# Performance work log

Hardware: AMD Instinct MI355X
Metric: run time of the kernel (lower is better)

## Reference

```python
import jax, jax.numpy as jnp
import numpy as np

TEMPERATURE = 0.07


def setup_inputs() -> dict:
    key = jax.random.key(0)
    k1, k2 = jax.random.split(key)
    B, D = 8192, 256
    embeddings = jax.random.normal(k1, (B, D), dtype=jnp.float32)
    ids = jax.random.randint(k2, (B,), 0, 1024, dtype=jnp.int64 if jax.config.jax_enable_x64 else jnp.int32)
    return {"embeddings": embeddings, "ids": ids}


def reference(embeddings, ids):
    B = embeddings.shape[0]
    # L2-normalize rows (F.normalize with p=2, dim=1)
    emb = embeddings / jnp.maximum(jnp.linalg.norm(embeddings, axis=1, keepdims=True), 1e-12)
    sim = (emb @ emb.T) / TEMPERATURE                      # [B, B]
    eye = jnp.eye(B, dtype=bool)
    sim = jnp.where(eye, -jnp.inf, sim)
    exp_sim = jnp.exp(sim)                                  # diag -> 0
    pos_mask = (ids[:, None] == ids[None, :]) & ~eye        # [B, B]
    pos_sum = jnp.sum(jnp.where(pos_mask, exp_sim, 0.0), axis=1)  # [B]
    all_sum = jnp.sum(exp_sim, axis=1)                      # [B]
    valid = pos_mask.any(axis=1)
    per_row = -jnp.log(pos_sum / all_sum)
    loss = jnp.sum(jnp.where(valid, per_row, 0.0))
    n_valid = jnp.sum(valid.astype(jnp.float32))
    return loss / jnp.maximum(n_valid, 1.0)
```

## Files before the change

### kernel.cpp

```cpp
#include <hip/hip_runtime.h>
#include <hip/hip_bf16.h>

#define B_SZ 8192
#define D_SZ 256
#define NTILES 2080
#define GRID_SIM 512
#define PRESCALE 4.539816004686735f

typedef __attribute__((ext_vector_type(4))) float f32x4;
typedef __attribute__((ext_vector_type(8))) short s16x8;

__global__ __launch_bounds__(256) void norm_kernel(const float* __restrict__ emb,
                                                   ushort* __restrict__ nbf,
                                                   float* __restrict__ sums) {
    sums[blockIdx.x * 64 + (threadIdx.x >> 2)] = 0.0f;

    const int wave = threadIdx.x >> 6, lane = threadIdx.x & 63;
    for (int g = blockIdx.x; g < B_SZ / 4; g += 256) {
        const int row = g * 4 + wave;
        const float4 v = ((const float4*)(emb + (size_t)row * D_SZ))[lane];
        float ss = v.x * v.x + v.y * v.y + v.z * v.z + v.w * v.w;
        #pragma unroll
        for (int m = 1; m < 64; m <<= 1) ss += __shfl_xor(ss, m, 64);
        float s = PRESCALE / fmaxf(sqrtf(ss), 1e-12f);
        __hip_bfloat16 b0 = __float2bfloat16(v.x * s);
        __hip_bfloat16 b1 = __float2bfloat16(v.y * s);
        __hip_bfloat16 b2 = __float2bfloat16(v.z * s);
        __hip_bfloat16 b3 = __float2bfloat16(v.w * s);
        ushort4 o;
        o.x = *(ushort*)&b0; o.y = *(ushort*)&b1; o.z = *(ushort*)&b2; o.w = *(ushort*)&b3;
        ((ushort4*)(nbf + (size_t)row * D_SZ))[lane] = o;
    }
}

__device__ __forceinline__ void decode_tile(int tb, int& i0, int& j0, bool& diag) {
    int bj = (int)((sqrtf(8.0f * tb + 1.0f) - 1.0f) * 0.5f);
    while ((bj + 1) * (bj + 2) / 2 <= tb) ++bj;
    while (bj * (bj + 1) / 2 > tb) --bj;
    const int bi = tb - bj * (bj + 1) / 2;
    i0 = bi * 128; j0 = bj * 128; diag = (bi == bj);
}

__device__ __forceinline__ void load_regs(s16x8 ra[4], s16x8 rb[4],
                                          const ushort* __restrict__ N,
                                          int i0, int j0, int k0,
                                          int wave, int r, int c8s) {
    const ushort* gA = N + (size_t)(i0 + wave * 32) * D_SZ + k0;
    const ushort* gB = N + (size_t)(j0 + wave * 32) * D_SZ + k0;
    #pragma unroll
    for (int q = 0; q < 4; ++q) {
        ra[q] = *(const s16x8*)(gA + (size_t)(q * 8 + r) * D_SZ + c8s);
        rb[q] = *(const s16x8*)(gB + (size_t)(q * 8 + r) * D_SZ + c8s);
    }
}

__device__ __forceinline__ void store_stage(const s16x8 ra[4], const s16x8 rb[4],
                                            ushort* bA, ushort* bB,
                                            int wave, int lane) {
    #pragma unroll
    for (int q = 0; q < 4; ++q) {
        *(s16x8*)&bA[(wave * 32 + q * 8) * 64 + lane * 8] = ra[q];
        *(s16x8*)&bB[(wave * 32 + q * 8) * 64 + lane * 8] = rb[q];
    }
}

__global__ __launch_bounds__(256) void sim_kernel(const ushort* __restrict__ N,
                                                  const int* __restrict__ ids,
                                                  float* __restrict__ all_sum,
                                                  float* __restrict__ pos_sum) {
    __shared__ ushort smem[4 * 128 * 64];

    const int t    = threadIdx.x;
    const int wave = t >> 6, lane = t & 63;
    const int wy   = wave >> 1, wx = wave & 1;
    const int r    = lane >> 3;
    const int c8s  = ((lane & 7) ^ r) * 8;
    const int myc  = lane & 15;

    int tb = blockIdx.x;
    int i0, j0; bool diag;
    decode_tile(tb, i0, j0, diag);

    s16x8 ra[4], rb[4];
    load_regs(ra, rb, N, i0, j0, 0, wave, r, c8s);

    while (true) {
        const int ntb = tb + GRID_SIM;
        const bool have_next = (ntb < NTILES);
        int ni0 = i0, nj0 = j0; bool ndiag = diag;
        if (have_next) decode_tile(ntb, ni0, nj0, ndiag);

        f32x4 acc[4][4];
        #pragma unroll
        for (int mi = 0; mi < 4; ++mi)
            #pragma unroll
            for (int ni = 0; ni < 4; ++ni)
                acc[mi][ni] = (f32x4){0.f, 0.f, 0.f, 0.f};

        #pragma unroll
        for (int kk = 0; kk < 4; ++kk) {
            ushort* bA = smem + (kk & 1) * 16384;
            ushort* bB = bA + 8192;
            store_stage(ra, rb, bA, bB, wave, lane);
            if (kk < 3)           load_regs(ra, rb, N, i0, j0, (kk + 1) * 64, wave, r, c8s);
            else if (have_next)   load_regs(ra, rb, N, ni0, nj0, 0, wave, r, c8s);
            __syncthreads();

            #pragma unroll
            for (int ks = 0; ks < 2; ++ks) {
                const int C = ks * 4 + (lane >> 4);
                const int slot = (C ^ (lane & 7)) * 8;
                s16x8 af[4], bf[4];
                #pragma unroll
                for (int mi = 0; mi < 4; ++mi)
                    af[mi] = *(const s16x8*)&bA[(wy * 64 + mi * 16 + (lane & 15)) * 64 + slot];
                #pragma unroll
                for (int ni = 0; ni < 4; ++ni)
                    bf[ni] = *(const s16x8*)&bB[(wx * 64 + ni * 16 + (lane & 15)) * 64 + slot];
                #pragma unroll
                for (int mi = 0; mi < 4; ++mi)
                    #pragma unroll
                    for (int ni = 0; ni < 4; ++ni)
                        acc[mi][ni] = __builtin_amdgcn_mfma_f32_16x16x32_bf16(
                            af[mi], bf[ni], acc[mi][ni], 0, 0, 0);
            }
        }

        float* rowAllPart = (float*)smem;
        float* rowPosPart = (float*)&smem[8192];

        int idc[4];
        #pragma unroll
        for (int ni = 0; ni < 4; ++ni)
            idc[ni] = ids[j0 + wx * 64 + ni * 16 + myc];

        float cAll[4] = {0.f, 0.f, 0.f, 0.f};
        float cPos[4] = {0.f, 0.f, 0.f, 0.f};

        #pragma unroll
        for (int mi = 0; mi < 4; ++mi) {
            float rAll[4] = {0.f, 0.f, 0.f, 0.f};
            float rPos[4] = {0.f, 0.f, 0.f, 0.f};
            const int rbase = wy * 64 + mi * 16 + (lane >> 4) * 4;
            const int4 idr  = *(const int4*)&ids[i0 + rbase];
            #pragma unroll
            for (int ni = 0; ni < 4; ++ni) {
                const int cloc = wx * 64 + ni * 16 + myc;
                #pragma unroll
                for (int rg = 0; rg < 4; ++rg) {
                    const int lr = rbase + rg;
                    float e = __builtin_amdgcn_exp2f(acc[mi][ni][rg]);
                    if (diag && lr == cloc) e = 0.0f;
                    rAll[rg] += e; cAll[ni] += e;
                    const int idrv = (rg == 0) ? idr.x : (rg == 1) ? idr.y
                                   : (rg == 2) ? idr.z : idr.w;
                    if (idrv == idc[ni]) { rPos[rg] += e; cPos[ni] += e; }
                }
            }
            #pragma unroll
            for (int rg = 0; rg < 4; ++rg) {
                rowAllPart[(rbase + rg) * 32 + wx * 16 + myc] = rAll[rg];
                rowPosPart[(rbase + rg) * 32 + wx * 16 + myc] = rPos[rg];
            }
        }

        if (!diag) {
            #pragma unroll
            for (int ni = 0; ni < 4; ++ni) {
                cAll[ni] += __shfl_xor(cAll[ni], 16, 64);
                cAll[ni] += __shfl_xor(cAll[ni], 32, 64);
                cPos[ni] += __shfl_xor(cPos[ni], 16, 64);
                cPos[ni] += __shfl_xor(cPos[ni], 32, 64);
            }
            if (lane < 16) {
                #pragma unroll
                for (int ni = 0; ni < 4; ++ni) {
                    const int gc = j0 + wx * 64 + ni * 16 + lane;
                    atomicAdd(&all_sum[gc], cAll[ni]);
                    if (cPos[ni] != 0.0f) atomicAdd(&pos_sum[gc], cPos[ni]);
                }
            }
        }

        __syncthreads();
        {
            const int row = t & 127;
            const float* src = (t >= 128) ? rowPosPart : rowAllPart;
            float s = 0.0f;
            #pragma unroll
            for (int k8 = 0; k8 < 8; ++k8) {
                const int chunk = (k8 + (row & 7)) & 7;
                const float4 v = *(const float4*)&src[row * 32 + chunk * 4];
                s += v.x + v.y + v.z + v.w;
            }
            float* dst = (t >= 128) ? pos_sum : all_sum;
            atomicAdd(&dst[i0 + row], s);
        }
        __syncthreads();

        if (!have_next) break;
        tb = ntb; i0 = ni0; j0 = nj0; diag = ndiag;
    }
}

__global__ __launch_bounds__(256) void loss_kernel(const float* __restrict__ all_sum,
                                                   const float* __restrict__ pos_sum,
                                                   float* __restrict__ out) {
    float loss = 0.0f, cnt = 0.0f;
    for (int i = threadIdx.x; i < B_SZ; i += 256) {
        float p = pos_sum[i], a = all_sum[i];
        if (p > 0.0f) { loss += logf(a) - logf(p); cnt += 1.0f; }
    }
    #pragma unroll
    for (int m = 1; m < 64; m <<= 1) {
        loss += __shfl_xor(loss, m, 64);
        cnt  += __shfl_xor(cnt, m, 64);
    }
    __shared__ float sl[4], sc[4];
    int wave = threadIdx.x >> 6, lane = threadIdx.x & 63;
    if (lane == 0) { sl[wave] = loss; sc[wave] = cnt; }
    __syncthreads();
    if (threadIdx.x == 0) {
        float L = sl[0] + sl[1] + sl[2] + sl[3];
        float C = sc[0] + sc[1] + sc[2] + sc[3];
        out[0] = L / fmaxf(C, 1.0f);
    }
}

extern "C" void kernel_launch(void* const* d_in, const int* in_sizes, int n_in,
                              void* d_out, int out_size, void* d_ws, size_t ws_size,
                              hipStream_t stream) {
    const float* emb = (const float*)d_in[0];
    const int*   ids = (const int*)d_in[1];
    float*       out = (float*)d_out;

    float*  all_sum = (float*)d_ws;
    float*  pos_sum = all_sum + B_SZ;
    ushort* nbf     = (ushort*)((char*)d_ws + 65536);

    norm_kernel<<<256, 256, 0, stream>>>(emb, nbf, all_sum);
    sim_kernel<<<GRID_SIM, 256, 0, stream>>>(nbf, ids, all_sum, pos_sum);
    loss_kernel<<<1, 256, 0, stream>>>(all_sum, pos_sum, out);
}
```

Before: 117.4 us.

## Shrink LDS stages to 32-wide K, deepen prefetch, and reduce rows via shuffles

The K loop now runs as eight 32-wide stages over a smaller double-buffered LDS region with a two-deep register prefetch, using a new XOR swizzle. The row-sum epilogue drops the LDS staging and its two block barriers; rows are instead reduced with wave shuffles and atomics from each half-wave. The grid doubles to 1024 blocks so more tiles run concurrently now that LDS use is lower. The cost is twice as many barriers per tile and more global atomics on the row sums.

Measured after the change: 182.4 us. 55.3% more time.

```diff
diff --git a/kernel.cpp b/kernel.cpp
--- a/kernel.cpp
+++ b/kernel.cpp
@@ -4,7 +4,7 @@
 #define B_SZ 8192
 #define D_SZ 256
 #define NTILES 2080
-#define GRID_SIM 512
+#define GRID_SIM 1024
 #define PRESCALE 4.539816004686735f
 
 typedef __attribute__((ext_vector_type(4))) float f32x4;
@@ -41,48 +41,74 @@
     i0 = bi * 128; j0 = bj * 128; diag = (bi == bj);
 }
 
-__device__ __forceinline__ void load_regs(s16x8 ra[4], s16x8 rb[4],
-                                          const ushort* __restrict__ N,
-                                          int i0, int j0, int k0,
-                                          int wave, int r, int c8s) {
-    const ushort* gA = N + (size_t)(i0 + wave * 32) * D_SZ + k0;
-    const ushort* gB = N + (size_t)(j0 + wave * 32) * D_SZ + k0;
-    #pragma unroll
-    for (int q = 0; q < 4; ++q) {
-        ra[q] = *(const s16x8*)(gA + (size_t)(q * 8 + r) * D_SZ + c8s);
-        rb[q] = *(const s16x8*)(gB + (size_t)(q * 8 + r) * D_SZ + c8s);
-    }
-}
-
-__device__ __forceinline__ void store_stage(const s16x8 ra[4], const s16x8 rb[4],
-                                            ushort* bA, ushort* bB,
-                                            int wave, int lane) {
-    #pragma unroll
-    for (int q = 0; q < 4; ++q) {
-        *(s16x8*)&bA[(wave * 32 + q * 8) * 64 + lane * 8] = ra[q];
-        *(s16x8*)&bB[(wave * 32 + q * 8) * 64 + lane * 8] = rb[q];
-    }
+__device__ __forceinline__ void load32(int4 ra[2], int4 rb[2],
+                                       const ushort* __restrict__ N,
+                                       int i0, int j0, int ke,
+                                       int wave, int lane) {
+    const int rbase = wave * 16 + (lane >> 2);
+    const int g     = lane & 3;
+    #pragma unroll
+    for (int h = 0; h < 2; ++h) {
+        const int row = rbase + h * 64;
+        ra[h] = *(const int4*)(N + (size_t)(i0 + row) * D_SZ + ke + g * 8);
+        rb[h] = *(const int4*)(N + (size_t)(j0 + row) * D_SZ + ke + g * 8);
+    }
+}
+
+__device__ __forceinline__ void store32(const int4 ra[2], const int4 rb[2],
+                                        ushort* bufA, ushort* bufB,
+                                        int wave, int lane) {
+    const int rbase = wave * 16 + (lane >> 2);
+    const int g     = lane & 3;
+    #pragma unroll
+    for (int h = 0; h < 2; ++h) {
+        const int row = rbase + h * 64;
+        const int s   = g ^ ((row >> 1) & 3);
+        *(int4*)&bufA[row * 32 + s * 8] = ra[h];
+        *(int4*)&bufB[row * 32 + s * 8] = rb[h];
+    }
+}
+
+__device__ __forceinline__ void compute32(const ushort* bufA, const ushort* bufB,
+                                          f32x4 acc[4][4], int wy, int wx, int lane) {
+    const int c16 = lane >> 4;
+    s16x8 af[4], bf[4];
+    #pragma unroll
+    for (int mi = 0; mi < 4; ++mi) {
+        const int rr = wy * 64 + mi * 16 + (lane & 15);
+        af[mi] = *(const s16x8*)&bufA[rr * 32 + (c16 ^ ((rr >> 1) & 3)) * 8];
+    }
+    #pragma unroll
+    for (int ni = 0; ni < 4; ++ni) {
+        const int rr = wx * 64 + ni * 16 + (lane & 15);
+        bf[ni] = *(const s16x8*)&bufB[rr * 32 + (c16 ^ ((rr >> 1) & 3)) * 8];
+    }
+    #pragma unroll
+    for (int mi = 0; mi < 4; ++mi)
+        #pragma unroll
+        for (int ni = 0; ni < 4; ++ni)
+            acc[mi][ni] = __builtin_amdgcn_mfma_f32_16x16x32_bf16(
+                af[mi], bf[ni], acc[mi][ni], 0, 0, 0);
 }
 
 __global__ __launch_bounds__(256) void sim_kernel(const ushort* __restrict__ N,
                                                   const int* __restrict__ ids,
                                                   float* __restrict__ all_sum,
                                                   float* __restrict__ pos_sum) {
-    __shared__ ushort smem[4 * 128 * 64];
+    __shared__ ushort smem[2 * 2 * 128 * 32];
 
     const int t    = threadIdx.x;
     const int wave = t >> 6, lane = t & 63;
     const int wy   = wave >> 1, wx = wave & 1;
-    const int r    = lane >> 3;
-    const int c8s  = ((lane & 7) ^ r) * 8;
     const int myc  = lane & 15;
 
     int tb = blockIdx.x;
     int i0, j0; bool diag;
     decode_tile(tb, i0, j0, diag);
 
-    s16x8 ra[4], rb[4];
-    load_regs(ra, rb, N, i0, j0, 0, wave, r, c8s);
+    int4 ra[2][2], rb[2][2];
+    load32(ra[0], rb[0], N, i0, j0, 0,  wave, lane);
+    load32(ra[1], rb[1], N, i0, j0, 32, wave, lane);
 
     while (true) {
         const int ntb = tb + GRID_SIM;
@@ -98,36 +124,18 @@
                 acc[mi][ni] = (f32x4){0.f, 0.f, 0.f, 0.f};
 
         #pragma unroll
-        for (int kk = 0; kk < 4; ++kk) {
-            ushort* bA = smem + (kk & 1) * 16384;
-            ushort* bB = bA + 8192;
-            store_stage(ra, rb, bA, bB, wave, lane);
-            if (kk < 3)           load_regs(ra, rb, N, i0, j0, (kk + 1) * 64, wave, r, c8s);
-            else if (have_next)   load_regs(ra, rb, N, ni0, nj0, 0, wave, r, c8s);
+        for (int kk = 0; kk < 8; ++kk) {
+            ushort* bufA = smem + (kk & 1) * 8192;
+            ushort* bufB = bufA + 4096;
+            const int s = kk & 1;
+            store32(ra[s], rb[s], bufA, bufB, wave, lane);
+            if (kk + 2 < 8)
+                load32(ra[s], rb[s], N, i0, j0, (kk + 2) * 32, wave, lane);
+            else if (have_next)
+                load32(ra[s], rb[s], N, ni0, nj0, (kk + 2 - 8) * 32, wave, lane);
             __syncthreads();
-
-            #pragma unroll
-            for (int ks = 0; ks < 2; ++ks) {
-                const int C = ks * 4 + (lane >> 4);
-                const int slot = (C ^ (lane & 7)) * 8;
-                s16x8 af[4], bf[4];
-                #pragma unroll
-                for (int mi = 0; mi < 4; ++mi)
-                    af[mi] = *(const s16x8*)&bA[(wy * 64 + mi * 16 + (lane & 15)) * 64 + slot];
-                #pragma unroll
-                for (int ni = 0; ni < 4; ++ni)
-                    bf[ni] = *(const s16x8*)&bB[(wx * 64 + ni * 16 + (lane & 15)) * 64 + slot];
-                #pragma unroll
-                for (int mi = 0; mi < 4; ++mi)
-                    #pragma unroll
-                    for (int ni = 0; ni < 4; ++ni)
-                        acc[mi][ni] = __builtin_amdgcn_mfma_f32_16x16x32_bf16(
-                            af[mi], bf[ni], acc[mi][ni], 0, 0, 0);
-            }
+            compute32(bufA, bufB, acc, wy, wx, lane);
         }
-
-        float* rowAllPart = (float*)smem;
-        float* rowPosPart = (float*)&smem[8192];
 
         int idc[4];
         #pragma unroll
@@ -148,9 +156,8 @@
                 const int cloc = wx * 64 + ni * 16 + myc;
                 #pragma unroll
                 for (int rg = 0; rg < 4; ++rg) {
-                    const int lr = rbase + rg;
                     float e = __builtin_amdgcn_exp2f(acc[mi][ni][rg]);
-                    if (diag && lr == cloc) e = 0.0f;
+                    if (diag && (rbase + rg) == cloc) e = 0.0f;
                     rAll[rg] += e; cAll[ni] += e;
                     const int idrv = (rg == 0) ? idr.x : (rg == 1) ? idr.y
                                    : (rg == 2) ? idr.z : idr.w;
@@ -159,8 +166,18 @@
             }
             #pragma unroll
             for (int rg = 0; rg < 4; ++rg) {
-                rowAllPart[(rbase + rg) * 32 + wx * 16 + myc] = rAll[rg];
-                rowPosPart[(rbase + rg) * 32 + wx * 16 + myc] = rPos[rg];
+                #pragma unroll
+                for (int mm = 1; mm < 16; mm <<= 1) {
+                    rAll[rg] += __shfl_xor(rAll[rg], mm, 64);
+                    rPos[rg] += __shfl_xor(rPos[rg], mm, 64);
+                }
+            }
+            if (myc == 0) {
+                #pragma unroll
+                for (int rg = 0; rg < 4; ++rg) {
+                    atomicAdd(&all_sum[i0 + rbase + rg], rAll[rg]);
+                    if (rPos[rg] != 0.0f) atomicAdd(&pos_sum[i0 + rbase + rg], rPos[rg]);
+                }
             }
         }
 
@@ -181,22 +198,6 @@
                 }
             }
         }
-
-        __syncthreads();
-        {
-            const int row = t & 127;
-            const float* src = (t >= 128) ? rowPosPart : rowAllPart;
-            float s = 0.0f;
-            #pragma unroll
-            for (int k8 = 0; k8 < 8; ++k8) {
-                const int chunk = (k8 + (row & 7)) & 7;
-                const float4 v = *(const float4*)&src[row * 32 + chunk * 4];
-                s += v.x + v.y + v.z + v.w;
-            }
-            float* dst = (t >= 128) ? pos_sum : all_sum;
-            atomicAdd(&dst[i0 + row], s);
-        }
-        __syncthreads();
 
         if (!have_next) break;
         tb = ntb; i0 = ni0; j0 = nj0; diag = ndiag;
```

## Single-buffer LDS, reduce row sums with shuffles, and double the grid

Applied to the files above, without the earlier changes.

Replaces the double-buffered shared memory with single A/B buffers plus an extra barrier per k-step, halving LDS use so more blocks can be resident. Row partial sums are now reduced with intra-wave shuffles and atomically added directly, instead of going through a shared-memory transpose and a second reduction pass with two barriers. The grid size doubles to 1024 to take advantage of the higher occupancy. The cost is an added sync per k-step and twice as many global atomics on row sums (one per wave-column half).

Result: slower. 130.5 us (+11.1%).

```diff
diff --git a/kernel.cpp b/kernel.cpp
--- a/kernel.cpp
+++ b/kernel.cpp
@@ -4,7 +4,7 @@
 #define B_SZ 8192
 #define D_SZ 256
 #define NTILES 2080
-#define GRID_SIM 512
+#define GRID_SIM 1024
 #define PRESCALE 4.539816004686735f
 
 typedef __attribute__((ext_vector_type(4))) float f32x4;
@@ -68,7 +68,8 @@
                                                   const int* __restrict__ ids,
                                                   float* __restrict__ all_sum,
                                                   float* __restrict__ pos_sum) {
-    __shared__ ushort smem[4 * 128 * 64];
+    __shared__ ushort sA[128 * 64];
+    __shared__ ushort sB[128 * 64];
 
     const int t    = threadIdx.x;
     const int wave = t >> 6, lane = t & 63;
@@ -99,9 +100,8 @@
 
         #pragma unroll
         for (int kk = 0; kk < 4; ++kk) {
-            ushort* bA = smem + (kk & 1) * 16384;
-            ushort* bB = bA + 8192;
-            store_stage(ra, rb, bA, bB, wave, lane);
+            __syncthreads();
+            store_stage(ra, rb, sA, sB, wave, lane);
             if (kk < 3)           load_regs(ra, rb, N, i0, j0, (kk + 1) * 64, wave, r, c8s);
             else if (have_next)   load_regs(ra, rb, N, ni0, nj0, 0, wave, r, c8s);
             __syncthreads();
@@ -113,10 +113,10 @@
                 s16x8 af[4], bf[4];
                 #pragma unroll
                 for (int mi = 0; mi < 4; ++mi)
-                    af[mi] = *(const s16x8*)&bA[(wy * 64 + mi * 16 + (lane & 15)) * 64 + slot];
+                    af[mi] = *(const s16x8*)&sA[(wy * 64 + mi * 16 + (lane & 15)) * 64 + slot];
                 #pragma unroll
                 for (int ni = 0; ni < 4; ++ni)
-                    bf[ni] = *(const s16x8*)&bB[(wx * 64 + ni * 16 + (lane & 15)) * 64 + slot];
+                    bf[ni] = *(const s16x8*)&sB[(wx * 64 + ni * 16 + (lane & 15)) * 64 + slot];
                 #pragma unroll
                 for (int mi = 0; mi < 4; ++mi)
                     #pragma unroll
@@ -126,9 +126,6 @@
             }
         }
 
-        float* rowAllPart = (float*)smem;
-        float* rowPosPart = (float*)&smem[8192];
-
         int idc[4];
         #pragma unroll
         for (int ni = 0; ni < 4; ++ni)
@@ -148,9 +145,8 @@
                 const int cloc = wx * 64 + ni * 16 + myc;
                 #pragma unroll
                 for (int rg = 0; rg < 4; ++rg) {
-                    const int lr = rbase + rg;
                     float e = __builtin_amdgcn_exp2f(acc[mi][ni][rg]);
-                    if (diag && lr == cloc) e = 0.0f;
+                    if (diag && (rbase + rg) == cloc) e = 0.0f;
                     rAll[rg] += e; cAll[ni] += e;
                     const int idrv = (rg == 0) ? idr.x : (rg == 1) ? idr.y
                                    : (rg == 2) ? idr.z : idr.w;
@@ -159,8 +155,18 @@
             }
             #pragma unroll
             for (int rg = 0; rg < 4; ++rg) {
-                rowAllPart[(rbase + rg) * 32 + wx * 16 + myc] = rAll[rg];
-                rowPosPart[(rbase + rg) * 32 + wx * 16 + myc] = rPos[rg];
+                #pragma unroll
+                for (int mm = 1; mm < 16; mm <<= 1) {
+                    rAll[rg] += __shfl_xor(rAll[rg], mm, 64);
+                    rPos[rg] += __shfl_xor(rPos[rg], mm, 64);
+                }
+            }
+            if (myc == 0) {
+                #pragma unroll
+                for (int rg = 0; rg < 4; ++rg) {
+                    atomicAdd(&all_sum[i0 + rbase + rg], rAll[rg]);
+                    if (rPos[rg] != 0.0f) atomicAdd(&pos_sum[i0 + rbase + rg], rPos[rg]);
+                }
             }
         }
 
@@ -181,22 +187,6 @@
                 }
             }
         }
-
-        __syncthreads();
-        {
-            const int row = t & 127;
-            const float* src = (t >= 128) ? rowPosPart : rowAllPart;
-            float s = 0.0f;
-            #pragma unroll
-            for (int k8 = 0; k8 < 8; ++k8) {
-                const int chunk = (k8 + (row & 7)) & 7;
-                const float4 v = *(const float4*)&src[row * 32 + chunk * 4];
-                s += v.x + v.y + v.z + v.w;
-            }
-            float* dst = (t >= 128) ? pos_sum : all_sum;
-            atomicAdd(&dst[i0 + row], s);
-        }
-        __syncthreads();
 
         if (!have_next) break;
         tb = ntb; i0 = ni0; j0 = nj0; diag = ndiag;
```
